# Kernel tuning notes

Hardware: AMD Instinct MI355X
Metric: run time of the kernel (lower is better)

The kernel has to match this reference:

```python
import jax, jax.numpy as jnp
import numpy as np

N_NODES = 10000
N_EDGES = 320000
CH = 64          # multiplicity per irrep (64x0e node feats)
R_DIM = 8        # radial embedding dim
L_MAX = 2
N_L = L_MAX + 1
SH_DIM = 9       # 1 + 3 + 5
AVG_NEIGH = 32.0
MLP_HID = 64


def setup_inputs() -> dict:
    key = jax.random.key(0)
    ks = jax.random.split(key, 11)
    return {
        "edge_vectors": jax.random.normal(ks[0], (N_EDGES, 3), jnp.float32),
        "node_feats": jax.random.normal(ks[1], (N_NODES, CH), jnp.float32),
        "radial_embeddings": jax.random.normal(ks[2], (N_EDGES, R_DIM), jnp.float32),
        "senders": jax.random.randint(ks[3], (N_EDGES,), 0, N_NODES),
        "receivers": jax.random.randint(ks[4], (N_EDGES,), 0, N_NODES),
        # learned params (e3nn Linear / MLP weights, unit normal init)
        "W_up": jax.random.normal(ks[5], (CH, CH), jnp.float32),
        "W_mlp1": jax.random.normal(ks[6], (R_DIM, MLP_HID), jnp.float32),
        "W_mlp2": jax.random.normal(ks[7], (MLP_HID, MLP_HID), jnp.float32),
        "W_mlp3": jax.random.normal(ks[8], (MLP_HID, MLP_HID), jnp.float32),
        "W_mlp4": jax.random.normal(ks[9], (MLP_HID, N_L * CH), jnp.float32),
        "W_down": jax.random.normal(ks[10], (N_L, CH, CH), jnp.float32),
    }


def spherical_harmonics(vec):
    """Component-normalized real spherical harmonics (||Y_l||^2 = 2l+1), l=0..2,
    on normalized edge vectors (e3nn normalize=True, normalization='component')."""
    v = vec / jnp.linalg.norm(vec, axis=-1, keepdims=True)
    x, y, z = v[..., 0], v[..., 1], v[..., 2]
    c15 = float(np.sqrt(15.0))
    c5 = float(np.sqrt(5.0))
    sh2 = jnp.stack(
        [c15 * x * y, c15 * y * z, 0.5 * c5 * (3.0 * z * z - 1.0),
         c15 * x * z, 0.5 * c15 * (x * x - y * y)], axis=-1)
    return jnp.concatenate(
        [jnp.ones_like(x)[..., None], float(np.sqrt(3.0)) * v, sh2], axis=-1)  # [E, 9]


def reference(edge_vectors, node_feats, radial_embeddings, senders, receivers,
              W_up, W_mlp1, W_mlp2, W_mlp3, W_mlp4, W_down):
    inv_ch = 1.0 / np.sqrt(CH)
    n_nodes = node_feats.shape[0]

    # linear_up: scalar irreps -> plain channel mixing with e3nn 1/sqrt(fan_in)
    h = (node_feats @ W_up) * inv_ch                               # [N, CH]

    sh = spherical_harmonics(edge_vectors)                         # [E, 9]

    # radial MLP -> one weight per (channel, l) tensor-product path
    m = radial_embeddings
    for W in (W_mlp1, W_mlp2, W_mlp3):
        m = jax.nn.silu((m @ W) / np.sqrt(W.shape[0]))
    mix = (m @ W_mlp4) / np.sqrt(MLP_HID)                          # [E, N_L*CH]
    w = mix.reshape(-1, N_L, CH).transpose(0, 2, 1)                # [E, CH, N_L]
    # broadcast each per-irrep weight over its 2l+1 components
    w = jnp.repeat(w, np.array([1, 3, 5]), axis=-1,
                   total_repeat_length=SH_DIM)                     # [E, CH, 9]

    # tensor product (scalar node feats x Y_l) with radial weights: messages
    msg = h[senders][:, :, None] * sh[:, None, :] * w              # [E, CH, 9]

    # scatter-add to receivers, normalize by avg_num_neighbors
    agg = jax.ops.segment_sum(msg.reshape(msg.shape[0], -1),
                              receivers, num_segments=n_nodes)
    agg = (agg / AVG_NEIGH).reshape(n_nodes, CH, SH_DIM)           # [N, CH, 9]

    # linear_down: independent channel mixing per l (equivariant Linear)
    outs = []
    start = 0
    for l in range(N_L):
        d = 2 * l + 1
        o = jnp.einsum('ncm,cd->ndm', agg[:, :, start:start + d], W_down[l]) * inv_ch
        outs.append(o.reshape(n_nodes, -1))
        start += d
    return jnp.concatenate(outs, axis=-1)                          # [N, 576]
```

## Files before the change

### kernel.cpp

```cpp
#include <hip/hip_runtime.h>
#include <hip/hip_bf16.h>
#include <math.h>

#define N_NODES 10000
#define N_EDGES 320000
#define CH 64
#define MIXW 192
#define EREC 12

#define W1_OFF 0
#define W2_OFF 512
#define W3_OFF 5120
#define W4_OFF 9728
#define W_TOT 23552
#define ACT_STRIDE 72

#define EPB 256

#define PREP_BLKS 92
#define H_BLKS 625
#define HIST_BLKS 1250

typedef __attribute__((ext_vector_type(8))) short bf16x8;
typedef __attribute__((ext_vector_type(4))) float f32x4;
#define MFMA16(a, b, c) __builtin_amdgcn_mfma_f32_16x16x32_bf16(a, b, c, 0, 0, 0)

__device__ __forceinline__ float bf2f(unsigned short u) {
    union { unsigned int i; float f; } v; v.i = ((unsigned int)u) << 16; return v.f;
}
__device__ __forceinline__ unsigned short f2bf(float f) {
    __hip_bfloat16 b = __float2bfloat16(f);
    return *reinterpret_cast<unsigned short*>(&b);
}
__device__ __forceinline__ float silu(float t) {
    return t * __builtin_amdgcn_rcpf(1.0f + __expf(-t));
}

__device__ __forceinline__ void load_bfrag(bf16x8 (&b)[4][2],
                                           const unsigned short* __restrict__ wbase,
                                           int lrow, int quad) {
#pragma unroll
    for (int nt = 0; nt < 4; ++nt)
#pragma unroll
        for (int kh = 0; kh < 2; ++kh)
            b[nt][kh] = *(const bf16x8*)(wbase + (nt * 16 + lrow) * 72 + kh * 32 + quad * 8);
}

__device__ __forceinline__ void layer64_t4(unsigned short* act, const bf16x8 (&b)[4][2],
                                           const int (&em)[4], const int (&cr)[4],
                                           int lrow, int quad) {
    bf16x8 a[4][2];
#pragma unroll
    for (int t = 0; t < 4; ++t) {
        a[t][0] = *(const bf16x8*)(act + em[t] * ACT_STRIDE + quad * 8);
        a[t][1] = *(const bf16x8*)(act + em[t] * ACT_STRIDE + 32 + quad * 8);
    }
#pragma unroll
    for (int nt = 0; nt < 4; ++nt) {
        f32x4 c[4];
#pragma unroll
        for (int t = 0; t < 4; ++t) {
            c[t] = (f32x4){0.f, 0.f, 0.f, 0.f};
            c[t] = MFMA16(a[t][0], b[nt][0], c[t]);
            c[t] = MFMA16(a[t][1], b[nt][1], c[t]);
        }
#pragma unroll
        for (int t = 0; t < 4; ++t)
#pragma unroll
            for (int r = 0; r < 4; ++r)
                act[(cr[t] + r) * ACT_STRIDE + nt * 16 + lrow] = f2bf(silu(c[t][r]));
    }
}

__device__ __forceinline__ void l4_third_t4(unsigned short* act,
                                            const int* s_pos,
                                            unsigned short* __restrict__ hw,
                                            const bf16x8 (&b)[4][2],
                                            const bf16x8 (&a)[4][2],
                                            const int (&cr)[4],
                                            int T, int wr0, int lane, int lrow, int quad) {
#pragma unroll
    for (int nt = 0; nt < 4; ++nt) {
        f32x4 c[4];
#pragma unroll
        for (int t = 0; t < 4; ++t) {
            c[t] = (f32x4){0.f, 0.f, 0.f, 0.f};
            c[t] = MFMA16(a[t][0], b[nt][0], c[t]);
            c[t] = MFMA16(a[t][1], b[nt][1], c[t]);
        }
#pragma unroll
        for (int t = 0; t < 4; ++t)
#pragma unroll
            for (int r = 0; r < 4; ++r)
                act[(cr[t] + r) * ACT_STRIDE + nt * 16 + lrow] = f2bf(c[t][r]);
    }
#pragma unroll
    for (int j = 0; j < 8; ++j) {
        int idx = lane + 64 * j;
        int row = idx >> 3, c8 = idx & 7;
        int p = s_pos[wr0 + row];
        uint4 v = *(const uint4*)(act + (wr0 + row) * ACT_STRIDE + c8 * 8);
        *(uint4*)(hw + (size_t)p * MIXW + T * 64 + c8 * 8) = v;
    }
}

__global__ __launch_bounds__(256) void k_pre(const float* __restrict__ W1,
                                             const float* __restrict__ W2,
                                             const float* __restrict__ W3,
                                             const float* __restrict__ W4,
                                             unsigned short* __restrict__ wimg,
                                             const float* __restrict__ nf,
                                             const float* __restrict__ Wup,
                                             float* __restrict__ h,
                                             const int* __restrict__ recv,
                                             int* __restrict__ counts) {
    int bid = blockIdx.x;
    int t = threadIdx.x;
    if (bid < PREP_BLKS) {
        int i = bid * 256 + t;
        if (i >= W_TOT) return;
        float v;
        if (i < W2_OFF) {
            int n = i >> 3, k = i & 7;
            v = W1[k * 64 + n] * 0.35355339059327376f;
        } else if (i < W3_OFF) {
            int j = i - W2_OFF; int n = j / 72, k = j % 72;
            v = (k < 64) ? W2[k * 64 + n] * 0.125f : 0.f;
        } else if (i < W4_OFF) {
            int j = i - W3_OFF; int n = j / 72, k = j % 72;
            v = (k < 64) ? W3[k * 64 + n] * 0.125f : 0.f;
        } else {
            int j = i - W4_OFF; int n = j / 72, k = j % 72;
            v = (k < 64) ? W4[k * MIXW + n] * 0.125f : 0.f;
        }
        wimg[i] = f2bf(v);
    } else if (bid < PREP_BLKS + H_BLKS) {
        int nb = __builtin_amdgcn_readfirstlane(
            (bid - PREP_BLKS) * 16 + (t >> 6) * 4);
        int lane = t & 63;
        const float* nrow = nf + (size_t)nb * CH;
        float a0 = 0.f, a1 = 0.f, a2 = 0.f, a3 = 0.f;
#pragma unroll
        for (int k = 0; k < CH; ++k) {
            float w = Wup[k * CH + lane];
            a0 = fmaf(nrow[k], w, a0);
            a1 = fmaf(nrow[CH + k], w, a1);
            a2 = fmaf(nrow[2 * CH + k], w, a2);
            a3 = fmaf(nrow[3 * CH + k], w, a3);
        }
        h[(size_t)nb * CH + lane] = a0 * 0.125f;
        h[(size_t)(nb + 1) * CH + lane] = a1 * 0.125f;
        h[(size_t)(nb + 2) * CH + lane] = a2 * 0.125f;
        h[(size_t)(nb + 3) * CH + lane] = a3 * 0.125f;
    } else {
        int e = (bid - PREP_BLKS - H_BLKS) * 256 + t;
        atomicAdd(&counts[recv[e]], 1);
    }
}

__global__ __launch_bounds__(1024) void k_scan(const int* __restrict__ counts,
                                               int* __restrict__ offsets,
                                               int* __restrict__ cursor) {
    __shared__ int wsum[16];
    int t = threadIdx.x;
    const int CHUNK = 10;
    int base = t * CHUNK;
    int s = 0;
    for (int i = 0; i < CHUNK; ++i) {
        int idx = base + i;
        if (idx < N_NODES) s += counts[idx];
    }
    int lane = t & 63, wv = t >> 6;
    int x = s;
#pragma unroll
    for (int off = 1; off < 64; off <<= 1) {
        int y = __shfl_up(x, off, 64);
        if (lane >= off) x += y;
    }
    if (lane == 63) wsum[wv] = x;
    __syncthreads();
    if (wv == 0 && lane < 16) {
        int v = wsum[lane];
#pragma unroll
        for (int off = 1; off < 16; off <<= 1) {
            int y = __shfl_up(v, off, 64);
            if (lane >= off) v += y;
        }
        wsum[lane] = v;
    }
    __syncthreads();
    int wbase = (wv == 0) ? 0 : wsum[wv - 1];
    int run = wbase + x - s;
    for (int i = 0; i < CHUNK; ++i) {
        int idx = base + i;
        if (idx < N_NODES) {
            offsets[idx] = run;
            cursor[idx] = run;
            run += counts[idx];
        }
    }
    if (t == 1023) offsets[N_NODES] = wbase + x;
}

__global__ __launch_bounds__(256) void k_mlp(const float* __restrict__ ev,
                                             const float* __restrict__ rad,
                                             const unsigned short* __restrict__ wimg,
                                             const int* __restrict__ senders,
                                             const int* __restrict__ recv,
                                             int* __restrict__ cursor,
                                             unsigned short* __restrict__ hw,
                                             float* __restrict__ erec) {
    __shared__ unsigned short act[EPB * ACT_STRIDE];
    __shared__ int s_pos[EPB];

    const int t = threadIdx.x;
    const int e0 = blockIdx.x * EPB;
    const int wv = t >> 6;
    const int lane = t & 63;
    const int lrow = lane & 15;
    const int quad = lane >> 4;
    const int wr0 = wv * 64;
    int em[4], cr[4];
#pragma unroll
    for (int tt = 0; tt < 4; ++tt) {
        em[tt] = wr0 + tt * 16 + lrow;
        cr[tt] = wr0 + tt * 16 + quad * 4;
    }

    bf16x8 ar[4];
    bf16x8 bw1[4];
#pragma unroll
    for (int nt = 0; nt < 4; ++nt) {
        ar[nt] = (bf16x8){0, 0, 0, 0, 0, 0, 0, 0};
        bw1[nt] = (bf16x8){0, 0, 0, 0, 0, 0, 0, 0};
    }
    bf16x8 bA[4][2], bB[4][2];
    load_bfrag(bA, wimg + W2_OFF, lrow, quad);
    if (quad == 0) {
#pragma unroll
        for (int tt = 0; tt < 4; ++tt) {
            const float4* rp0 = (const float4*)(rad + (size_t)(e0 + em[tt]) * 8);
            float4 u = rp0[0], v = rp0[1];
            ar[tt][0] = (short)f2bf(u.x); ar[tt][1] = (short)f2bf(u.y);
            ar[tt][2] = (short)f2bf(u.z); ar[tt][3] = (short)f2bf(u.w);
            ar[tt][4] = (short)f2bf(v.x); ar[tt][5] = (short)f2bf(v.y);
            ar[tt][6] = (short)f2bf(v.z); ar[tt][7] = (short)f2bf(v.w);
        }
#pragma unroll
        for (int nt = 0; nt < 4; ++nt)
            bw1[nt] = *(const bf16x8*)(wimg + W1_OFF + (nt * 16 + lrow) * 8);
    }

    {
        int e = e0 + wr0 + lane;
        int p = atomicAdd(&cursor[recv[e]], 1);
        s_pos[wr0 + lane] = p;
        int snd = senders[e];
        float vx = ev[(size_t)e * 3 + 0], vy = ev[(size_t)e * 3 + 1], vz = ev[(size_t)e * 3 + 2];
        float inv = rsqrtf(vx * vx + vy * vy + vz * vz);
        float x = vx * inv, y = vy * inv, z = vz * inv;
        const float s3 = 1.7320508075688772f;
        const float s15 = 3.872983346207417f;
        const float s5 = 2.2360679774997896f;
        float4* rp = (float4*)(erec + (size_t)p * EREC);
        rp[0] = make_float4(1.0f, s3 * x, s3 * y, s3 * z);
        rp[1] = make_float4(s15 * x * y, s15 * y * z, 0.5f * s5 * (3.0f * z * z - 1.0f), s15 * x * z);
        rp[2] = make_float4(0.5f * s15 * (x * x - y * y), __int_as_float(snd), 0.f, 0.f);
    }

#pragma unroll
    for (int nt = 0; nt < 4; ++nt) {
        f32x4 c[4];
#pragma unroll
        for (int tt = 0; tt < 4; ++tt) {
            c[tt] = (f32x4){0.f, 0.f, 0.f, 0.f};
            c[tt] = MFMA16(ar[tt], bw1[nt], c[tt]);
        }
#pragma unroll
        for (int tt = 0; tt < 4; ++tt)
#pragma unroll
            for (int r = 0; r < 4; ++r)
                act[(cr[tt] + r) * ACT_STRIDE + nt * 16 + lrow] = f2bf(silu(c[tt][r]));
    }

    load_bfrag(bB, wimg + W3_OFF, lrow, quad);
    layer64_t4(act, bA, em, cr, lrow, quad);

    load_bfrag(bA, wimg + W4_OFF, lrow, quad);
    layer64_t4(act, bB, em, cr, lrow, quad);

    {
        bf16x8 a[4][2];
#pragma unroll
        for (int tt = 0; tt < 4; ++tt) {
            a[tt][0] = *(const bf16x8*)(act + em[tt] * ACT_STRIDE + quad * 8);
            a[tt][1] = *(const bf16x8*)(act + em[tt] * ACT_STRIDE + 32 + quad * 8);
        }
        load_bfrag(bB, wimg + W4_OFF + 64 * 72, lrow, quad);
        l4_third_t4(act, s_pos, hw, bA, a, cr, 0, wr0, lane, lrow, quad);
        load_bfrag(bA, wimg + W4_OFF + 2 * 64 * 72, lrow, quad);
        l4_third_t4(act, s_pos, hw, bB, a, cr, 1, wr0, lane, lrow, quad);
        l4_third_t4(act, s_pos, hw, bA, a, cr, 2, wr0, lane, lrow, quad);
    }
}

__global__ __launch_bounds__(256, 4) void k_aggdown(const int* __restrict__ offsets,
                                                    const float* __restrict__ erec,
                                                    const unsigned short* __restrict__ hw,
                                                    const float* __restrict__ h,
                                                    const float* __restrict__ Wd,
                                                    float* __restrict__ out) {
    __shared__ float sg[4][576];
    int wv = threadIdx.x >> 6;
    int lane = threadIdx.x & 63;
    int node = __builtin_amdgcn_readfirstlane(blockIdx.x * 4 + wv);
    int s0 = __builtin_amdgcn_readfirstlane(offsets[node]);
    int s1 = __builtin_amdgcn_readfirstlane(offsets[node + 1]);
    float acc[9] = {0.f, 0.f, 0.f, 0.f, 0.f, 0.f, 0.f, 0.f, 0.f};
#pragma unroll 4
    for (int i = s0; i < s1; ++i) {
        const float* rp = erec + (size_t)i * EREC;
        const unsigned short* hrow = hw + (size_t)i * MIXW;
        int snd = __float_as_int(rp[9]);
        float hh = h[(size_t)snd * CH + lane];
        float w0 = bf2f(hrow[lane]) * hh;
        float w1 = bf2f(hrow[64 + lane]) * hh;
        float w2 = bf2f(hrow[128 + lane]) * hh;
        acc[0] += w0 * rp[0];
        acc[1] += w1 * rp[1];
        acc[2] += w1 * rp[2];
        acc[3] += w1 * rp[3];
        acc[4] += w2 * rp[4];
        acc[5] += w2 * rp[5];
        acc[6] += w2 * rp[6];
        acc[7] += w2 * rp[7];
        acc[8] += w2 * rp[8];
    }
    float* arow = sg[wv];
#pragma unroll
    for (int m = 0; m < 9; ++m) arow[lane * 9 + m] = acc[m] * (1.0f / 32.0f);

    float* orow = out + (size_t)node * 576;
    {
        float a = 0.f;
#pragma unroll
        for (int c = 0; c < 64; ++c) a += arow[c * 9] * Wd[c * 64 + lane];
        orow[lane] = a * 0.125f;
    }
    {
        float m3[3] = {0.f, 0.f, 0.f};
#pragma unroll
        for (int c = 0; c < 64; ++c) {
            float w = Wd[(64 + c) * 64 + lane];
#pragma unroll
            for (int mm = 0; mm < 3; ++mm) m3[mm] += arow[c * 9 + 1 + mm] * w;
        }
#pragma unroll
        for (int mm = 0; mm < 3; ++mm) orow[64 + lane * 3 + mm] = m3[mm] * 0.125f;
    }
    {
        float m5[5] = {0.f, 0.f, 0.f, 0.f, 0.f};
#pragma unroll
        for (int c = 0; c < 64; ++c) {
            float w = Wd[(128 + c) * 64 + lane];
#pragma unroll
            for (int mm = 0; mm < 5; ++mm) m5[mm] += arow[c * 9 + 4 + mm] * w;
        }
#pragma unroll
        for (int mm = 0; mm < 5; ++mm) orow[256 + lane * 5 + mm] = m5[mm] * 0.125f;
    }
}

static inline size_t align256(size_t x) { return (x + 255) & ~(size_t)255; }

extern "C" void kernel_launch(void* const* d_in, const int* in_sizes, int n_in,
                              void* d_out, int out_size, void* d_ws, size_t ws_size,
                              hipStream_t stream) {
    const float* edge_vectors = (const float*)d_in[0];
    const float* node_feats   = (const float*)d_in[1];
    const float* radial       = (const float*)d_in[2];
    const int*   senders      = (const int*)d_in[3];
    const int*   receivers    = (const int*)d_in[4];
    const float* W_up         = (const float*)d_in[5];
    const float* W_mlp1       = (const float*)d_in[6];
    const float* W_mlp2       = (const float*)d_in[7];
    const float* W_mlp3       = (const float*)d_in[8];
    const float* W_mlp4       = (const float*)d_in[9];
    const float* W_down       = (const float*)d_in[10];
    float* out = (float*)d_out;

    char* base = (char*)d_ws;
    size_t off = 0;
    float* h = (float*)(base + off);              off = align256(off + (size_t)N_NODES * CH * 4);
    unsigned short* hw = (unsigned short*)(base + off); off = align256(off + (size_t)N_EDGES * MIXW * 2);
    float* erec = (float*)(base + off);           off = align256(off + (size_t)N_EDGES * EREC * 4);
    unsigned short* wimg = (unsigned short*)(base + off); off = align256(off + (size_t)W_TOT * 2);
    int* counts = (int*)(base + off);             off = align256(off + (size_t)N_NODES * 4);
    int* offsets = (int*)(base + off);            off = align256(off + (size_t)(N_NODES + 1) * 4);
    int* cursor = (int*)(base + off);             off = align256(off + (size_t)N_NODES * 4);

    hipMemsetAsync(counts, 0, (size_t)N_NODES * 4, stream);

    k_pre<<<PREP_BLKS + H_BLKS + HIST_BLKS, 256, 0, stream>>>(
        W_mlp1, W_mlp2, W_mlp3, W_mlp4, wimg, node_feats, W_up, h, receivers, counts);
    k_scan<<<1, 1024, 0, stream>>>(counts, offsets, cursor);
    k_mlp<<<N_EDGES / EPB, 256, 0, stream>>>(edge_vectors, radial, wimg, senders,
                                             receivers, cursor, hw, erec);
    k_aggdown<<<N_NODES / 4, 256, 0, stream>>>(offsets, erec, hw, h, W_down, out);
}
```

Measured before the change: 219.3 us.

## Fold sender feature gather into MLP epilogue, pad edge records to 16 floats

```diff
diff --git a/kernel.cpp b/kernel.cpp
--- a/kernel.cpp
+++ b/kernel.cpp
@@ -6,7 +6,7 @@
 #define N_EDGES 320000
 #define CH 64
 #define MIXW 192
-#define EREC 12
+#define EREC 16
 
 #define W1_OFF 0
 #define W2_OFF 512
@@ -77,6 +77,7 @@
                                             unsigned short* __restrict__ hw,
                                             const bf16x8 (&b)[4][2],
                                             const bf16x8 (&a)[4][2],
+                                            const float (&hreg)[4][4][4],
                                             const int (&cr)[4],
                                             int T, int wr0, int lane, int lrow, int quad) {
 #pragma unroll
@@ -92,7 +93,8 @@
         for (int t = 0; t < 4; ++t)
 #pragma unroll
             for (int r = 0; r < 4; ++r)
-                act[(cr[t] + r) * ACT_STRIDE + nt * 16 + lrow] = f2bf(c[t][r]);
+                act[(cr[t] + r) * ACT_STRIDE + nt * 16 + lrow] =
+                    f2bf(c[t][r] * hreg[t][r][nt]);
     }
 #pragma unroll
     for (int j = 0; j < 8; ++j) {
@@ -208,10 +210,12 @@
                                              const int* __restrict__ senders,
                                              const int* __restrict__ recv,
                                              int* __restrict__ cursor,
+                                             const float* __restrict__ h,
                                              unsigned short* __restrict__ hw,
                                              float* __restrict__ erec) {
     __shared__ unsigned short act[EPB * ACT_STRIDE];
     __shared__ int s_pos[EPB];
+    __shared__ int s_snd[EPB];
 
     const int t = threadIdx.x;
     const int e0 = blockIdx.x * EPB;
@@ -255,7 +259,7 @@
         int e = e0 + wr0 + lane;
         int p = atomicAdd(&cursor[recv[e]], 1);
         s_pos[wr0 + lane] = p;
-        int snd = senders[e];
+        s_snd[wr0 + lane] = senders[e];
         float vx = ev[(size_t)e * 3 + 0], vy = ev[(size_t)e * 3 + 1], vz = ev[(size_t)e * 3 + 2];
         float inv = rsqrtf(vx * vx + vy * vy + vz * vz);
         float x = vx * inv, y = vy * inv, z = vz * inv;
@@ -265,7 +269,8 @@
         float4* rp = (float4*)(erec + (size_t)p * EREC);
         rp[0] = make_float4(1.0f, s3 * x, s3 * y, s3 * z);
         rp[1] = make_float4(s15 * x * y, s15 * y * z, 0.5f * s5 * (3.0f * z * z - 1.0f), s15 * x * z);
-        rp[2] = make_float4(0.5f * s15 * (x * x - y * y), __int_as_float(snd), 0.f, 0.f);
+        rp[2] = make_float4(0.5f * s15 * (x * x - y * y), 0.f, 0.f, 0.f);
+        rp[3] = make_float4(0.f, 0.f, 0.f, 0.f);
     }
 
 #pragma unroll
@@ -287,7 +292,24 @@
     layer64_t4(act, bA, em, cr, lrow, quad);
 
     load_bfrag(bA, wimg + W4_OFF, lrow, quad);
+    int sn[4][4];
+#pragma unroll
+    for (int tt = 0; tt < 4; ++tt)
+#pragma unroll
+        for (int r = 0; r < 4; ++r)
+            sn[tt][r] = s_snd[cr[tt] + r];
     layer64_t4(act, bB, em, cr, lrow, quad);
+
+    float hreg[4][4][4];
+#pragma unroll
+    for (int tt = 0; tt < 4; ++tt)
+#pragma unroll
+        for (int r = 0; r < 4; ++r) {
+            const float* hb = h + (size_t)sn[tt][r] * CH + lrow;
+#pragma unroll
+            for (int nt = 0; nt < 4; ++nt)
+                hreg[tt][r][nt] = hb[nt * 16];
+        }
 
     {
         bf16x8 a[4][2];
@@ -297,17 +319,16 @@
             a[tt][1] = *(const bf16x8*)(act + em[tt] * ACT_STRIDE + 32 + quad * 8);
         }
         load_bfrag(bB, wimg + W4_OFF + 64 * 72, lrow, quad);
-        l4_third_t4(act, s_pos, hw, bA, a, cr, 0, wr0, lane, lrow, quad);
+        l4_third_t4(act, s_pos, hw, bA, a, hreg, cr, 0, wr0, lane, lrow, quad);
         load_bfrag(bA, wimg + W4_OFF + 2 * 64 * 72, lrow, quad);
-        l4_third_t4(act, s_pos, hw, bB, a, cr, 1, wr0, lane, lrow, quad);
-        l4_third_t4(act, s_pos, hw, bA, a, cr, 2, wr0, lane, lrow, quad);
+        l4_third_t4(act, s_pos, hw, bB, a, hreg, cr, 1, wr0, lane, lrow, quad);
+        l4_third_t4(act, s_pos, hw, bA, a, hreg, cr, 2, wr0, lane, lrow, quad);
     }
 }
 
 __global__ __launch_bounds__(256, 4) void k_aggdown(const int* __restrict__ offsets,
                                                     const float* __restrict__ erec,
                                                     const unsigned short* __restrict__ hw,
-                                                    const float* __restrict__ h,
                                                     const float* __restrict__ Wd,
                                                     float* __restrict__ out) {
     __shared__ float sg[4][576];
@@ -317,15 +338,13 @@
     int s0 = __builtin_amdgcn_readfirstlane(offsets[node]);
     int s1 = __builtin_amdgcn_readfirstlane(offsets[node + 1]);
     float acc[9] = {0.f, 0.f, 0.f, 0.f, 0.f, 0.f, 0.f, 0.f, 0.f};
-#pragma unroll 4
+#pragma unroll 8
     for (int i = s0; i < s1; ++i) {
         const float* rp = erec + (size_t)i * EREC;
         const unsigned short* hrow = hw + (size_t)i * MIXW;
-        int snd = __float_as_int(rp[9]);
-        float hh = h[(size_t)snd * CH + lane];
-        float w0 = bf2f(hrow[lane]) * hh;
-        float w1 = bf2f(hrow[64 + lane]) * hh;
-        float w2 = bf2f(hrow[128 + lane]) * hh;
+        float w0 = bf2f(hrow[lane]);
+        float w1 = bf2f(hrow[64 + lane]);
+        float w2 = bf2f(hrow[128 + lane]);
         acc[0] += w0 * rp[0];
         acc[1] += w1 * rp[1];
         acc[2] += w1 * rp[2];
@@ -405,6 +424,6 @@
         W_mlp1, W_mlp2, W_mlp3, W_mlp4, wimg, node_feats, W_up, h, receivers, counts);
     k_scan<<<1, 1024, 0, stream>>>(counts, offsets, cursor);
     k_mlp<<<N_EDGES / EPB, 256, 0, stream>>>(edge_vectors, radial, wimg, senders,
-                                             receivers, cursor, hw, erec);
-    k_aggdown<<<N_NODES / 4, 256, 0, stream>>>(offsets, erec, hw, h, W_down, out);
-}
+                                             receivers, cursor, h, hw, erec);
+    k_aggdown<<<N_NODES / 4, 256, 0, stream>>>(offsets, erec, hw, W_down, out);
+}
```

Result: faster. 213.1 us (-2.8%).
